# Performance work log

Hardware: AMD Instinct MI355X
Metric: run time of the kernel (lower is better)

The kernel has to match this reference:

```python
import jax, jax.numpy as jnp
import numpy as np

INPUT_DIM, ENC_H, DEC_H, HORIZON = 8, 384, 384, 18
B, L = 1024, 336


def _lstm_layer(xs, Wih, Whh, bih, bhh):
    # xs: [B, L, D] -> outputs [B, L, H], final h [B, H]
    Bv = xs.shape[0]
    Hh = Whh.shape[1]
    def step(carry, x_t):
        h, c = carry
        z = x_t @ Wih.T + h @ Whh.T + bih + bhh  # [B, 4H], gate order i,f,g,o (PyTorch)
        i, f, g, o = jnp.split(z, 4, axis=-1)
        c = jax.nn.sigmoid(f) * c + jax.nn.sigmoid(i) * jnp.tanh(g)
        h = jax.nn.sigmoid(o) * jnp.tanh(c)
        return (h, c), h
    init = (jnp.zeros((Bv, Hh), xs.dtype), jnp.zeros((Bv, Hh), xs.dtype))
    (h, c), ys = jax.lax.scan(step, init, jnp.swapaxes(xs, 0, 1))
    return jnp.swapaxes(ys, 0, 1), h


def setup_inputs() -> dict:
    key = jax.random.key(0)
    ks = jax.random.split(key, 20)
    s = 0.05
    d = {
        "x": jax.random.normal(ks[0], (B, L, INPUT_DIM), jnp.float32),
        "future_feats": jax.random.normal(ks[1], (B, HORIZON, 4), jnp.float32),
        # encoder layer 0
        "enc_Wih0": jax.random.normal(ks[2], (4 * ENC_H, INPUT_DIM), jnp.float32) * s,
        "enc_Whh0": jax.random.normal(ks[3], (4 * ENC_H, ENC_H), jnp.float32) * s,
        "enc_bih0": jax.random.normal(ks[4], (4 * ENC_H,), jnp.float32) * s,
        "enc_bhh0": jax.random.normal(ks[5], (4 * ENC_H,), jnp.float32) * s,
        # encoder layer 1
        "enc_Wih1": jax.random.normal(ks[6], (4 * ENC_H, ENC_H), jnp.float32) * s,
        "enc_Whh1": jax.random.normal(ks[7], (4 * ENC_H, ENC_H), jnp.float32) * s,
        "enc_bih1": jax.random.normal(ks[8], (4 * ENC_H,), jnp.float32) * s,
        "enc_bhh1": jax.random.normal(ks[9], (4 * ENC_H,), jnp.float32) * s,
        # attention projection (no bias)
        "Wa": jax.random.normal(ks[10], (DEC_H, ENC_H), jnp.float32) * s,
        # dec_in: Linear(1+4+enc_h -> dec_h)
        "dec_in_W": jax.random.normal(ks[11], (DEC_H, 1 + 4 + ENC_H), jnp.float32) * s,
        "dec_in_b": jax.random.normal(ks[12], (DEC_H,), jnp.float32) * s,
        # decoder LSTM (1 layer)
        "dec_Wih": jax.random.normal(ks[13], (4 * DEC_H, DEC_H), jnp.float32) * s,
        "dec_Whh": jax.random.normal(ks[14], (4 * DEC_H, DEC_H), jnp.float32) * s,
        "dec_bih": jax.random.normal(ks[15], (4 * DEC_H,), jnp.float32) * s,
        "dec_bhh": jax.random.normal(ks[16], (4 * DEC_H,), jnp.float32) * s,
        # output head
        "out_W": jax.random.normal(ks[17], (1, DEC_H), jnp.float32) * s,
        "out_b": jax.random.normal(ks[18], (1,), jnp.float32) * s,
    }
    return d


def reference(x, future_feats, enc_Wih0, enc_Whh0, enc_bih0, enc_bhh0,
              enc_Wih1, enc_Whh1, enc_bih1, enc_bhh1, Wa, dec_in_W, dec_in_b,
              dec_Wih, dec_Whh, dec_bih, dec_bhh, out_W, out_b):
    Bv = x.shape[0]
    # 2-layer encoder (eval mode: inter-layer dropout inactive)
    h1, _ = _lstm_layer(x, enc_Wih0, enc_Whh0, enc_bih0, enc_bhh0)
    enc_out, h_last = _lstm_layer(h1, enc_Wih1, enc_Whh1, enc_bih1, enc_bhh1)
    proj = enc_out @ Wa.T  # [B, L, dec_h] (Wa(enc_out) is step-invariant)

    def dec_step(carry, feat_t):
        h, c, y_prev = carry
        scores = jnp.einsum('bld,bd->bl', proj, h)
        alpha = jax.nn.softmax(scores, axis=1)
        ctx = jnp.einsum('bl,bld->bd', alpha, enc_out)
        din = jnp.concatenate([y_prev, feat_t, ctx], axis=1)  # [B, 1+4+enc_h]
        din = jax.nn.relu(din @ dec_in_W.T + dec_in_b)
        z = din @ dec_Wih.T + h @ dec_Whh.T + dec_bih + dec_bhh
        i, f, g, o = jnp.split(z, 4, axis=-1)
        c = jax.nn.sigmoid(f) * c + jax.nn.sigmoid(i) * jnp.tanh(g)
        h = jax.nn.sigmoid(o) * jnp.tanh(c)
        y_t = h @ out_W.T + out_b  # [B, 1]
        y_prev = jax.lax.stop_gradient(y_t)  # .detach() in torch
        return (h, c, y_prev), y_t

    init = (h_last, jnp.zeros_like(h_last), jnp.zeros((Bv, 1), x.dtype))
    _, ys = jax.lax.scan(dec_step, init, jnp.swapaxes(future_feats, 0, 1))
    return jnp.swapaxes(ys, 0, 1)  # [B, horizon, 1]
```

## Files before the change

kernel.cpp:

```cpp
#include <hip/hip_runtime.h>
#include <stdint.h>

typedef __bf16 bf16;
typedef __bf16 bf16x8 __attribute__((ext_vector_type(8)));
typedef short  s16x8  __attribute__((ext_vector_type(8)));
typedef float  f32x4  __attribute__((ext_vector_type(4)));
typedef uint32_t u32;

#define NB   1024
#define LSEQ 336
#define HID  384
#define HOR  18
#define SMEM_BYTES 36864

__device__ bf16  g_H0[(size_t)(LSEQ+1)*NB*HID];
__device__ bf16  g_enc[(size_t)NB*LSEQ*HID];
__device__ bf16  g_zero[HID];
__device__ bf16  g_Adec[2*NB*768];
__device__ bf16  g_Adin[NB*416];
__device__ bf16  g_xb[NB*LSEQ*8];
__device__ float g_cdec[NB*HID];
__device__ float g_u[NB*HID];
__device__ float g_bias0[1536], g_bias1[1536], g_biasd[1536], g_biasdin[384];
__device__ bf16  g_Bp0[12*13*4096];
__device__ bf16  g_Bp1n[24*24*4*64*8];
__device__ bf16  g_Bpd[12*24*4096];
__device__ bf16  g_Bpi[3*13*4096];
__device__ bf16  g_Bpu[3*12*4096];
__device__ int   g_f0[8*LSEQ];
__device__ int   g_f1[4*(LSEQ+1)];

__device__ __forceinline__ float sigf(float x){ return 1.0f/(1.0f + __expf(-x)); }
__device__ __forceinline__ float tanh_f(float x){
  x = fminf(fmaxf(x, -15.f), 15.f);
  float e = __expf(2.f*x);
  return (e - 1.f)/(e + 1.f);
}

__device__ __forceinline__ void ds16(bf16* p, s16x8 v){
  union{ s16x8 v; uint64_t q[2]; } u; u.v = v;
  __hip_atomic_store((uint64_t*)p,     u.q[0], __ATOMIC_RELAXED, __HIP_MEMORY_SCOPE_AGENT);
  __hip_atomic_store((uint64_t*)p + 1, u.q[1], __ATOMIC_RELAXED, __HIP_MEMORY_SCOPE_AGENT);
}

__global__ void zero_state_k(){
  int i = blockIdx.x*blockDim.x + threadIdx.x;
  int st = gridDim.x*blockDim.x;
  bf16 z = (bf16)0.f;
  for(int k=i;k<NB*HID;k+=st){ g_H0[k]=z; g_cdec[k]=0.f; }
  for(int k=i;k<8*LSEQ;k+=st) g_f0[k]=0;
  for(int k=i;k<4*(LSEQ+1);k+=st) g_f1[k]=0;
}

__global__ void pack_xb_k(const float* __restrict__ x){
  int i = blockIdx.x*256 + threadIdx.x;
  int n = NB*LSEQ*8;
  for(int k=i; k<n; k+=gridDim.x*256) g_xb[k] = (bf16)x[k];
}

__global__ void pack_gates_k(int mode, const float* __restrict__ W1, const float* __restrict__ W2,
                             int nks){
  bf16* out = (mode==0)? g_Bp0 : g_Bpd;
  size_t idx = (size_t)blockIdx.x*256 + threadIdx.x;
  size_t total = (size_t)12*nks*512;
  if(idx >= total) return;
  int lane = (int)(idx & 63);
  int tt   = (int)((idx>>6) & 7);
  size_t tmp = idx >> 9;
  int ks = (int)(tmp % nks);
  int jb = (int)(tmp / nks);
  int n  = (tt>>1)*HID + jb*32 + (tt&1)*16 + (lane&15);
  int kb = ks*32 + (lane>>4)*8;
  bf16x8 v;
  #pragma unroll
  for(int i=0;i<8;i++){
    int k = kb + i;
    float f;
    if(mode==0) f = (k<384) ? W1[(size_t)n*384 + k] : (k<392 ? W2[(size_t)n*8 + (k-384)] : 0.f);
    else        f = (k<384) ? W1[(size_t)n*384 + k] : W2[(size_t)n*384 + (k-384)];
    v[i] = (bf16)f;
  }
  *(bf16x8*)(out + idx*8) = v;
}

__global__ void pack_gates16_k(const float* __restrict__ Wih1, const float* __restrict__ Whh1){
  int idx = blockIdx.x*256 + threadIdx.x;
  if(idx >= 24*24*4*64) return;
  int lane = idx&63, rem = idx>>6;
  int g = rem&3; rem >>= 2;
  int ks = rem%24, jn = rem/24;
  int n  = g*HID + jn*16 + (lane&15);
  int kb = ks*32 + (lane>>4)*8;
  bf16x8 v;
  #pragma unroll
  for(int i=0;i<8;i++){
    int k = kb+i;
    float f = (k<384)? Wih1[(size_t)n*384 + k] : Whh1[(size_t)n*384 + (k-384)];
    v[i] = (bf16)f;
  }
  *(bf16x8*)(g_Bp1n + (size_t)idx*8) = v;
}

__global__ void pack_plain_k(int mode, const float* __restrict__ W, int nks, int nb_cnt){
  bf16* out = mode ? g_Bpu : g_Bpi;
  size_t idx = (size_t)blockIdx.x*256 + threadIdx.x;
  size_t total = (size_t)nb_cnt*nks*512;
  if(idx>=total) return;
  int lane = (int)(idx&63);
  int tt   = (int)((idx>>6)&7);
  size_t tmp = idx>>9;
  int ks = (int)(tmp%nks);
  int nb = (int)(tmp/nks);
  int n  = nb*128 + tt*16 + (lane&15);
  int kb = ks*32 + (lane>>4)*8;
  bf16x8 v;
  #pragma unroll
  for(int i=0;i<8;i++){
    int k = kb+i;
    float f;
    if(mode==0) f = (k<389)? W[(size_t)n*389 + k] : 0.f;
    else        f = W[(size_t)k*384 + n];
    v[i]=(bf16)f;
  }
  *(bf16x8*)(out + idx*8) = v;
}

__global__ void prep_misc_k(const float* bih0,const float* bhh0,const float* bih1,const float* bhh1,
                            const float* dbih,const float* dbhh,const float* dinb){
  int i = blockIdx.x*256 + threadIdx.x;
  if(i<1536){ g_bias0[i]=bih0[i]+bhh0[i]; g_bias1[i]=bih1[i]+bhh1[i]; g_biasd[i]=dbih[i]+dbhh[i]; }
  if(i<384) g_biasdin[i]=dinb[i];
}

__device__ __forceinline__ void spin_ge(int* p, int tgt){
  while(__hip_atomic_load(p, __ATOMIC_RELAXED, __HIP_MEMORY_SCOPE_AGENT) < tgt){}
}

__global__ __launch_bounds__(256,1)
void enc7_k(){
  extern __shared__ char lds[];
  const int bid = blockIdx.x, tid = threadIdx.x;
  const int lane = tid&63, wv = tid>>6;
  const int l15 = lane&15, lk = (lane>>4)*8;

  if(bid < 96){
    const int g = bid & 7, jb = bid >> 3;
    { const s16x8* src = (const s16x8*)(g_Bp0 + (size_t)jb*13*4096);
      s16x8* dst = (s16x8*)lds;
      #pragma unroll
      for(int h=0;h<26;h++) dst[tid + h*256] = src[tid + h*256];
    }
    bf16* tr = (bf16*)(lds + 13*8192);
    __syncthreads();
    const int jj0 = jb*32 + l15;
    float bia[2],bfa[2],bga[2],boa[2];
    #pragma unroll
    for(int jh=0;jh<2;jh++){
      bia[jh]=g_bias0[jj0+jh*16];     bfa[jh]=g_bias0[384+jj0+jh*16];
      bga[jh]=g_bias0[768+jj0+jh*16]; boa[jh]=g_bias0[1152+jj0+jh*16];
    }
    size_t hoff[2], xoff[2];
    #pragma unroll
    for(int mt=0;mt<2;mt++){
      int row = g*128 + wv*32 + mt*16 + l15;
      hoff[mt] = (size_t)row*HID + lk;
      xoff[mt] = (size_t)row*LSEQ*8;
    }
    float c[2][2][4] = {};
    for(int w=0; w<LSEQ; w++){
      if(tid==0 && w>=1) spin_ge(&g_f0[g*LSEQ + (w-1)], 12);
      __syncthreads();
      asm volatile("" ::: "memory");
      const bf16* H0w = g_H0 + (size_t)w*NB*HID;
      bf16x8 af[13][2];
      #pragma unroll
      for(int ks=0;ks<12;ks++)
        #pragma unroll
        for(int mt=0;mt<2;mt++)
          af[ks][mt] = *(const bf16x8*)(H0w + hoff[mt] + ks*32);
      #pragma unroll
      for(int mt=0;mt<2;mt++){
        bf16x8 z;
        #pragma unroll
        for(int e=0;e<8;e++) z[e]=(bf16)0.f;
        if(lk==0) z = *(const bf16x8*)(g_xb + xoff[mt] + (size_t)w*8);
        af[12][mt] = z;
      }
      f32x4 acc[2][8];
      #pragma unroll
      for(int m2=0;m2<2;m2++)
        #pragma unroll
        for(int tt=0;tt<8;tt++) acc[m2][tt] = (f32x4){0.f,0.f,0.f,0.f};
      #pragma unroll
      for(int ks=0;ks<13;ks++){
        #pragma unroll
        for(int tt=0;tt<8;tt++){
          bf16x8 bfr = *(const bf16x8*)(lds + (ks*8+tt)*1024 + lane*16);
          acc[0][tt] = __builtin_amdgcn_mfma_f32_16x16x32_bf16(af[ks][0], bfr, acc[0][tt],0,0,0);
          acc[1][tt] = __builtin_amdgcn_mfma_f32_16x16x32_bf16(af[ks][1], bfr, acc[1][tt],0,0,0);
        }
      }
      #pragma unroll
      for(int mt=0;mt<2;mt++)
        #pragma unroll
        for(int jh=0;jh<2;jh++)
          #pragma unroll
          for(int r=0;r<4;r++){
            float zi=acc[mt][0+jh][r]+bia[jh], zf=acc[mt][2+jh][r]+bfa[jh],
                  zg=acc[mt][4+jh][r]+bga[jh], zo=acc[mt][6+jh][r]+boa[jh];
            float cn = sigf(zf)*c[mt][jh][r] + sigf(zi)*tanh_f(zg);
            c[mt][jh][r]=cn;
            int lr = wv*32 + mt*16 + (lane>>4)*4 + r;
            tr[lr*32 + jh*16 + l15] = (bf16)(sigf(zo)*tanh_f(cn));
          }
      __syncthreads();
      bf16* H0n = g_H0 + (size_t)(w+1)*NB*HID;
      #pragma unroll
      for(int h=0;h<2;h++){
        int p = tid + h*256;
        int row = p>>2, cc = p&3;
        s16x8 v = *(const s16x8*)(tr + row*32 + cc*8);
        ds16(H0n + (size_t)(g*128+row)*HID + jb*32 + cc*8, v);
      }
      __syncthreads();
      if(tid==0)
        __hip_atomic_fetch_add(&g_f0[g*LSEQ + w], 1, __ATOMIC_RELAXED, __HIP_MEMORY_SCOPE_AGENT);
    }
  } else {
    const int idx = bid-96, m = idx & 3, jn = idx >> 2;
    { const s16x8* src = (const s16x8*)(g_Bp1n + (size_t)jn*24*2048);
      s16x8* dst = (s16x8*)lds;
      #pragma unroll
      for(int h=0;h<24;h++) dst[tid + h*256] = src[tid + h*256];
    }
    bf16* tr = (bf16*)(lds + 24*4096);
    __syncthreads();
    const int jj = jn*16 + l15;
    const float bi=g_bias1[jj], bff=g_bias1[384+jj], bg=g_bias1[768+jj], bo=g_bias1[1152+jj];
    int rows[4]; size_t hoff[4];
    #pragma unroll
    for(int mt=0;mt<4;mt++){
      rows[mt] = m*256 + wv*64 + mt*16 + l15;
      hoff[mt] = (size_t)rows[mt]*HID + lk;
    }
    float c[4][4] = {};
    for(int s=1; s<=LSEQ; s++){
      if(tid==0)           spin_ge(&g_f0[(2*m)*LSEQ + (s-1)], 12);
      else if(tid==1)      spin_ge(&g_f0[(2*m+1)*LSEQ + (s-1)], 12);
      else if(tid==2 && s>=2) spin_ge(&g_f1[m*(LSEQ+1) + (s-1)], 24);
      __syncthreads();
      asm volatile("" ::: "memory");
      const bf16* H0s = g_H0 + (size_t)s*NB*HID;
      const size_t strideE = (s>=2)? (size_t)LSEQ*HID : 0;
      const bf16* Es = (s>=2)? (g_enc + (size_t)(s-2)*HID) : g_zero;
      size_t eoff[4];
      #pragma unroll
      for(int mt=0;mt<4;mt++) eoff[mt] = (size_t)rows[mt]*strideE + lk;
      bf16x8 ap[8][4];
      #pragma unroll
      for(int d=0; d<8; d++)
        #pragma unroll
        for(int mt=0;mt<4;mt++)
          ap[d][mt] = *(const bf16x8*)(H0s + hoff[mt] + d*32);
      f32x4 acc[4][4];
      #pragma unroll
      for(int mt=0;mt<4;mt++)
        #pragma unroll
        for(int g4=0;g4<4;g4++) acc[mt][g4] = (f32x4){0.f,0.f,0.f,0.f};
      #pragma unroll
      for(int ks=0;ks<24;ks++){
        bf16x8 bfr[4];
        #pragma unroll
        for(int g4=0;g4<4;g4++) bfr[g4] = *(const bf16x8*)(lds + (ks*4+g4)*1024 + lane*16);
        bf16x8 a[4];
        #pragma unroll
        for(int mt=0;mt<4;mt++) a[mt] = ap[ks&7][mt];
        int kn = ks+8;
        if(kn<24){
          if(kn<12){
            #pragma unroll
            for(int mt=0;mt<4;mt++) ap[ks&7][mt] = *(const bf16x8*)(H0s + hoff[mt] + kn*32);
          } else {
            #pragma unroll
            for(int mt=0;mt<4;mt++) ap[ks&7][mt] = *(const bf16x8*)(Es + eoff[mt] + (kn-12)*32);
          }
        }
        #pragma unroll
        for(int mt=0;mt<4;mt++)
          #pragma unroll
          for(int g4=0;g4<4;g4++)
            acc[mt][g4] = __builtin_amdgcn_mfma_f32_16x16x32_bf16(a[mt], bfr[g4], acc[mt][g4],0,0,0);
      }
      #pragma unroll
      for(int mt=0;mt<4;mt++)
        #pragma unroll
        for(int r=0;r<4;r++){
          float zi=acc[mt][0][r]+bi, zf=acc[mt][1][r]+bff,
                zg=acc[mt][2][r]+bg, zo=acc[mt][3][r]+bo;
          float cn = sigf(zf)*c[mt][r] + sigf(zi)*tanh_f(zg);
          c[mt][r]=cn;
          int lr = wv*64 + mt*16 + (lane>>4)*4 + r;
          tr[lr*16 + l15] = (bf16)(sigf(zo)*tanh_f(cn));
        }
      __syncthreads();
      const int t = s-1;
      #pragma unroll
      for(int h=0;h<2;h++){
        int p = tid + h*256;
        int row = p>>1, hf2 = p&1;
        s16x8 v = *(const s16x8*)(tr + row*16 + hf2*8);
        ds16(g_enc + ((size_t)(m*256+row)*LSEQ + t)*HID + jn*16 + hf2*8, v);
      }
      __syncthreads();
      if(tid==0)
        __hip_atomic_fetch_add(&g_f1[m*(LSEQ+1) + s], 1, __ATOMIC_RELAXED, __HIP_MEMORY_SCOPE_AGENT);
    }
  }
}

struct SReg { s16x8 a0,a1,b0,b1; };

__device__ __forceinline__ void stage_load(const bf16* __restrict__ A, int ldA,
                                           const bf16* __restrict__ Bk, int tid, SReg& sr){
  int c0 = tid, c1 = tid+256;
  sr.a0 = *(const s16x8*)(A + (size_t)(c0>>2)*ldA + (c0&3)*8);
  sr.a1 = *(const s16x8*)(A + (size_t)(c1>>2)*ldA + (c1&3)*8);
  const s16x8* B8 = (const s16x8*)Bk;
  sr.b0 = B8[c0]; sr.b1 = B8[c1];
}

__device__ __forceinline__ void stage_write(char* Ab, char* Bb, int tid, const SReg& sr){
  int c0 = tid, c1 = tid+256;
  *(s16x8*)(Ab + (c0>>2)*80 + (c0&3)*16) = sr.a0;
  *(s16x8*)(Ab + (c1>>2)*80 + (c1&3)*16) = sr.a1;
  *(s16x8*)(Bb + c0*16) = sr.b0;
  *(s16x8*)(Bb + c1*16) = sr.b1;
}

__device__ __forceinline__ void gemm_core(const bf16* __restrict__ A, int ldA,
                                          const bf16* __restrict__ Bp, int nks,
                                          char* smem, f32x4 acc[4][4]){
  const int tid = threadIdx.x;
  const int lane = tid & 63, wv = tid>>6, wm = wv>>1, wn = wv&1;
  char* Ab0 = smem;            char* Ab1 = smem + 10240;
  char* Bb0 = smem + 20480;    char* Bb1 = smem + 28672;
  f32x4 z = {0.f,0.f,0.f,0.f};
  #pragma unroll
  for(int m=0;m<4;m++)
    #pragma unroll
    for(int g=0;g<4;g++) acc[m][g]=z;
  SReg sr;
  stage_load(A, ldA, Bp, tid, sr);
  stage_write(Ab0, Bb0, tid, sr);
  const int aoff = (wm*64 + (lane&15))*80 + (lane>>4)*16;
  const int boff = wn*1024 + lane*16;
  for(int ks=0; ks<nks; ks++){
    char* Ac = (ks&1)? Ab1: Ab0;
    char* Bc = (ks&1)? Bb1: Bb0;
    char* An = (ks&1)? Ab0: Ab1;
    char* Bn = (ks&1)? Bb0: Bb1;
    bool more = (ks+1)<nks;
    if(more) stage_load(A + (ks+1)*32, ldA, Bp + (size_t)(ks+1)*4096, tid, sr);
    __syncthreads();
    bf16x8 af[4], bfr[4];
    #pragma unroll
    for(int mt=0;mt<4;mt++) af[mt] = *(const bf16x8*)(Ac + aoff + mt*16*80);
    #pragma unroll
    for(int g=0;g<4;g++)    bfr[g] = *(const bf16x8*)(Bc + boff + g*2048);
    #pragma unroll
    for(int mt=0;mt<4;mt++)
      #pragma unroll
      for(int g=0;g<4;g++)
        acc[mt][g] = __builtin_amdgcn_mfma_f32_16x16x32_bf16(af[mt], bfr[g], acc[mt][g], 0,0,0);
    if(more) stage_write(An, Bn, tid, sr);
  }
}

__device__ __forceinline__ void lstm_epi(f32x4 acc[4][4], int mbase, int jb,
     const float* __restrict__ bias, float* __restrict__ cst,
     bf16* __restrict__ d0, int ld0, bf16* __restrict__ d1, size_t ld1){
  int lane = threadIdx.x&63, wv = threadIdx.x>>6, wm = wv>>1, wn = wv&1;
  int j = jb*32 + wn*16 + (lane&15);
  float bi = bias[j], bff = bias[384+j], bg = bias[768+j], bo = bias[1152+j];
  #pragma unroll
  for(int mt=0;mt<4;mt++){
    #pragma unroll
    for(int r=0;r<4;r++){
      int brow = mbase + wm*64 + mt*16 + (lane>>4)*4 + r;
      float zi = acc[mt][0][r]+bi, zf = acc[mt][1][r]+bff,
            zg = acc[mt][2][r]+bg, zo = acc[mt][3][r]+bo;
      size_t ci = (size_t)brow*HID + j;
      float cold = cst[ci];
      float cn = sigf(zf)*cold + sigf(zi)*tanh_f(zg);
      cst[ci] = cn;
      bf16 hb = (bf16)(sigf(zo)*tanh_f(cn));
      d0[(size_t)brow*ld0 + j] = hb;
      if(d1) d1[(size_t)brow*ld1 + j] = hb;
    }
  }
}

__global__ __launch_bounds__(256)
void dec_lstm_k(int t){
  __shared__ char smem[SMEM_BYTES];
  int bid = blockIdx.x, mb = bid/12, jb = bid%12;
  int rs = t&1, wsl = rs^1;
  f32x4 acc[4][4];
  gemm_core(g_Adec + (size_t)rs*NB*768 + (size_t)mb*128*768, 768,
            g_Bpd + (size_t)jb*24*4096, 24, smem, acc);
  lstm_epi(acc, mb*128, jb, g_biasd, g_cdec,
           g_Adec + (size_t)wsl*NB*768 + 384, 768, (bf16*)nullptr, 0);
}

__global__ __launch_bounds__(256)
void plain_gemm_k(int t, int mode, const float* __restrict__ outW,
                  const float* __restrict__ outb, float* __restrict__ out,
                  const float* __restrict__ ff){
  __shared__ char smem[SMEM_BYTES];
  int bid = blockIdx.x, mb = bid/3, nb = bid%3;
  int rs = t&1;
  const bf16* A; int ldA, nks; const bf16* Bp;
  if(mode==1){ A = g_Adec + (size_t)rs*NB*768 + 384; ldA=768; Bp = g_Bpu; nks=12; }
  else       { A = g_Adin;                           ldA=416; Bp = g_Bpi; nks=13; }
  f32x4 acc[4][4];
  gemm_core(A + (size_t)mb*128*ldA, ldA, Bp + (size_t)nb*nks*4096, nks, smem, acc);
  int lane = threadIdx.x&63, wv = threadIdx.x>>6, wm = wv>>1, wn = wv&1;
  bf16* dbf = g_Adec + (size_t)rs*NB*768;
  #pragma unroll
  for(int mt=0;mt<4;mt++){
    #pragma unroll
    for(int ti=0;ti<4;ti++){
      int n = nb*128 + (ti*2+wn)*16 + (lane&15);
      #pragma unroll
      for(int r=0;r<4;r++){
        int brow = mb*128 + wm*64 + mt*16 + (lane>>4)*4 + r;
        float v = acc[mt][ti][r];
        if(mode==0){ v += g_biasdin[n]; v = fmaxf(v,0.f); dbf[(size_t)brow*768 + n] = (bf16)v; }
        else g_u[(size_t)brow*384 + n] = v;
      }
    }
  }
  if(mode==1 && t>=1 && nb==0 && threadIdx.x<128){
    int b = mb*128 + threadIdx.x;
    const s16x8* hp = (const s16x8*)(g_Adec + (size_t)rs*NB*768 + (size_t)b*768 + 384);
    float acc2 = 0.f;
    #pragma unroll 4
    for(int i=0;i<48;i++){
      s16x8 v = hp[i];
      #pragma unroll
      for(int e=0;e<8;e++){
        float hv = __uint_as_float(((u32)(uint16_t)v[e])<<16);
        acc2 += hv*outW[i*8+e];
      }
    }
    float y = acc2 + outb[0];
    out[(size_t)b*HOR + (t-1)] = y;
    g_Adin[(size_t)b*416] = (bf16)y;
    #pragma unroll
    for(int k=0;k<4;k++) g_Adin[(size_t)b*416 + 1 + k] = (bf16)ff[(size_t)b*HOR*4 + t*4 + k];
  }
}

__global__ __launch_bounds__(256)
void attn_k(int t){
  __shared__ float sm[4][392];
  int tid = threadIdx.x, lane = tid&63, w = tid>>6;
  int bl = w>>1, hf = w&1;
  int b = blockIdx.x*2 + bl;
  const float* ub = g_u + (size_t)b*HID + lane*6;
  float u0=ub[0],u1=ub[1],u2=ub[2],u3=ub[3],u4=ub[4],u5=ub[5];
  const u32* er = (const u32*)(g_enc + (size_t)b*LSEQ*HID) + (size_t)hf*168*192 + lane*3;
  int estep = 192;
  if(t & 1){ er += (size_t)167*192; estep = -192; }
  float m=-1e30f, den=0.f, a0=0,a1=0,a2=0,a3=0,a4=0,a5=0;
  for(int l=0;l<168;l++){
    u32 w0 = er[0], w1 = er[1], w2 = er[2];
    er += estep;
    float e0 = __uint_as_float(w0<<16);
    float e1 = __uint_as_float(w0 & 0xffff0000u);
    float e2 = __uint_as_float(w1<<16);
    float e3 = __uint_as_float(w1 & 0xffff0000u);
    float e4 = __uint_as_float(w2<<16);
    float e5 = __uint_as_float(w2 & 0xffff0000u);
    float p = e0*u0 + e1*u1 + e2*u2 + e3*u3 + e4*u4 + e5*u5;
    #pragma unroll
    for(int o=1;o<64;o<<=1) p += __shfl_xor(p, o, 64);
    float mn = fmaxf(m, p);
    float al = __expf(m - mn), pe = __expf(p - mn);
    den = den*al + pe;
    a0 = a0*al + pe*e0; a1 = a1*al + pe*e1; a2 = a2*al + pe*e2;
    a3 = a3*al + pe*e3; a4 = a4*al + pe*e4; a5 = a5*al + pe*e5;
    m = mn;
  }
  if(lane==0){ sm[w][0]=m; sm[w][1]=den; }
  sm[w][2+lane*6+0]=a0; sm[w][2+lane*6+1]=a1; sm[w][2+lane*6+2]=a2;
  sm[w][2+lane*6+3]=a3; sm[w][2+lane*6+4]=a4; sm[w][2+lane*6+5]=a5;
  __syncthreads();
  if(hf==0){
    float m2 = sm[w+1][0], d2 = sm[w+1][1];
    float M = fmaxf(m, m2);
    float f1 = __expf(m - M), f2 = __expf(m2 - M);
    float inv = 1.f/(den*f1 + d2*f2);
    bf16* cd = g_Adin + (size_t)b*416 + 5 + lane*6;
    cd[0] = (bf16)((a0*f1 + sm[w+1][2+lane*6+0]*f2)*inv);
    cd[1] = (bf16)((a1*f1 + sm[w+1][2+lane*6+1]*f2)*inv);
    cd[2] = (bf16)((a2*f1 + sm[w+1][2+lane*6+2]*f2)*inv);
    cd[3] = (bf16)((a3*f1 + sm[w+1][2+lane*6+3]*f2)*inv);
    cd[4] = (bf16)((a4*f1 + sm[w+1][2+lane*6+4]*f2)*inv);
    cd[5] = (bf16)((a5*f1 + sm[w+1][2+lane*6+5]*f2)*inv);
  }
}

__global__ void post_k(int t, const float* __restrict__ outW,
                       const float* __restrict__ outb, float* __restrict__ out){
  int b = blockIdx.x*256 + threadIdx.x;
  if(b>=NB) return;
  int wsl = (t&1)^1;
  const s16x8* hp = (const s16x8*)(g_Adec + (size_t)wsl*NB*768 + (size_t)b*768 + 384);
  float acc = 0.f;
  #pragma unroll 4
  for(int i=0;i<48;i++){
    s16x8 v = hp[i];
    #pragma unroll
    for(int e=0;e<8;e++){
      float hv = __uint_as_float(((u32)(uint16_t)v[e])<<16);
      acc += hv*outW[i*8+e];
    }
  }
  out[(size_t)b*HOR + t] = acc + outb[0];
}

__global__ void dec_prep_k(const float* __restrict__ ff){
  int i = blockIdx.x*256 + threadIdx.x;
  if(i < NB*HID){
    int b = i/HID, j = i%HID;
    g_Adec[(size_t)b*768 + 384 + j] = g_enc[(size_t)b*LSEQ*HID + (size_t)(LSEQ-1)*HID + j];
  }
  if(i < NB*4){
    int b = i>>2, k = i&3;
    g_Adin[(size_t)b*416 + 1 + k] = (bf16)ff[(size_t)b*HOR*4 + k];
  }
  if(i < NB) g_Adin[(size_t)i*416] = (bf16)0.f;
}

extern "C" void kernel_launch(void* const* d_in, const int* in_sizes, int n_in,
                              void* d_out, int out_size, void* d_ws, size_t ws_size,
                              hipStream_t stream){
  const float* x    = (const float*)d_in[0];
  const float* ff   = (const float*)d_in[1];
  const float* Wih0 = (const float*)d_in[2];
  const float* Whh0 = (const float*)d_in[3];
  const float* bih0 = (const float*)d_in[4];
  const float* bhh0 = (const float*)d_in[5];
  const float* Wih1 = (const float*)d_in[6];
  const float* Whh1 = (const float*)d_in[7];
  const float* bih1 = (const float*)d_in[8];
  const float* bhh1 = (const float*)d_in[9];
  const float* Wa   = (const float*)d_in[10];
  const float* dinW = (const float*)d_in[11];
  const float* dinb = (const float*)d_in[12];
  const float* dWih = (const float*)d_in[13];
  const float* dWhh = (const float*)d_in[14];
  const float* dbih = (const float*)d_in[15];
  const float* dbhh = (const float*)d_in[16];
  const float* outW = (const float*)d_in[17];
  const float* outb = (const float*)d_in[18];
  float* out = (float*)d_out;

  zero_state_k<<<1024,256,0,stream>>>();
  pack_xb_k<<<2048,256,0,stream>>>(x);
  pack_gates_k<<<(12*13*512)/256,256,0,stream>>>(0, Whh0, Wih0, 13);
  pack_gates16_k<<<576,256,0,stream>>>(Wih1, Whh1);
  pack_gates_k<<<(12*24*512)/256,256,0,stream>>>(2, dWih, dWhh, 24);
  pack_plain_k<<<(3*13*512)/256,256,0,stream>>>(0, dinW, 13, 3);
  pack_plain_k<<<(3*12*512)/256,256,0,stream>>>(1, Wa, 12, 3);
  prep_misc_k<<<8,256,0,stream>>>(bih0,bhh0,bih1,bhh1,dbih,dbhh,dinb);

  hipFuncSetAttribute((const void*)enc7_k,
                      hipFuncAttributeMaxDynamicSharedMemorySize, 114688);
  enc7_k<<<192,256,114688,stream>>>();

  dec_prep_k<<<1536,256,0,stream>>>(ff);
  for(int t=0;t<HOR;t++){
    plain_gemm_k<<<24,256,0,stream>>>(t, 1, outW, outb, out, ff);
    attn_k<<<512,256,0,stream>>>(t);
    plain_gemm_k<<<24,256,0,stream>>>(t, 0, outW, outb, out, ff);
    dec_lstm_k<<<96,256,0,stream>>>(t);
  }
  post_k<<<4,256,0,stream>>>(17, outW, outb, out);
  (void)in_sizes; (void)n_in; (void)out_size; (void)d_ws; (void)ws_size;
}
```

Baseline: 8.402 ms.

## Stage layer-1 encoder state in compact per-step buffer and overlap dependency wait

Layer-1 hidden outputs are now written to a step-indexed, column-slab-major buffer (g_E1), so the recurrent operand reads of the next step are contiguous instead of strided across the sequence-major g_enc. Blocks copy the previous step's slab into g_enc off the critical path, and the last step is copied after the loop. The wait on the layer-1 flag now happens after the layer-0 operand prefetch, letting those loads overlap the wait. Per-store atomic 64-bit writes are replaced by plain vector stores plus an agent-scope release fence before the flag increment. This adds an extra copy and a large staging buffer, and relies on the fence to keep ordering correct.

```diff
diff --git a/kernel.cpp b/kernel.cpp
--- a/kernel.cpp
+++ b/kernel.cpp
@@ -12,10 +12,11 @@
 #define HID  384
 #define HOR  18
 #define SMEM_BYTES 36864
+#define E1T  ((size_t)24*NB*16)
 
 __device__ bf16  g_H0[(size_t)(LSEQ+1)*NB*HID];
+__device__ bf16  g_E1[(size_t)(LSEQ+1)*E1T];
 __device__ bf16  g_enc[(size_t)NB*LSEQ*HID];
-__device__ bf16  g_zero[HID];
 __device__ bf16  g_Adec[2*NB*768];
 __device__ bf16  g_Adin[NB*416];
 __device__ bf16  g_xb[NB*LSEQ*8];
@@ -37,17 +38,11 @@
   return (e - 1.f)/(e + 1.f);
 }
 
-__device__ __forceinline__ void ds16(bf16* p, s16x8 v){
-  union{ s16x8 v; uint64_t q[2]; } u; u.v = v;
-  __hip_atomic_store((uint64_t*)p,     u.q[0], __ATOMIC_RELAXED, __HIP_MEMORY_SCOPE_AGENT);
-  __hip_atomic_store((uint64_t*)p + 1, u.q[1], __ATOMIC_RELAXED, __HIP_MEMORY_SCOPE_AGENT);
-}
-
 __global__ void zero_state_k(){
   int i = blockIdx.x*blockDim.x + threadIdx.x;
   int st = gridDim.x*blockDim.x;
   bf16 z = (bf16)0.f;
-  for(int k=i;k<NB*HID;k+=st){ g_H0[k]=z; g_cdec[k]=0.f; }
+  for(int k=i;k<NB*HID;k+=st){ g_H0[k]=z; g_E1[k]=z; g_cdec[k]=0.f; }
   for(int k=i;k<8*LSEQ;k+=st) g_f0[k]=0;
   for(int k=i;k<4*(LSEQ+1);k+=st) g_f1[k]=0;
 }
@@ -135,9 +130,12 @@
 __device__ __forceinline__ void spin_ge(int* p, int tgt){
   while(__hip_atomic_load(p, __ATOMIC_RELAXED, __HIP_MEMORY_SCOPE_AGENT) < tgt){}
 }
+__device__ __forceinline__ void release_agent(){
+  __builtin_amdgcn_fence(__ATOMIC_RELEASE, "agent");
+}
 
 __global__ __launch_bounds__(256,1)
-void enc7_k(){
+void enc8_k(){
   extern __shared__ char lds[];
   const int bid = blockIdx.x, tid = threadIdx.x;
   const int lane = tid&63, wv = tid>>6;
@@ -220,11 +218,13 @@
         int p = tid + h*256;
         int row = p>>2, cc = p&3;
         s16x8 v = *(const s16x8*)(tr + row*32 + cc*8);
-        ds16(H0n + (size_t)(g*128+row)*HID + jb*32 + cc*8, v);
+        *(s16x8*)(H0n + (size_t)(g*128+row)*HID + jb*32 + cc*8) = v;
       }
       __syncthreads();
-      if(tid==0)
+      if(tid==0){
+        release_agent();
         __hip_atomic_fetch_add(&g_f0[g*LSEQ + w], 1, __ATOMIC_RELAXED, __HIP_MEMORY_SCOPE_AGENT);
+      }
     }
   } else {
     const int idx = bid-96, m = idx & 3, jn = idx >> 2;
@@ -237,31 +237,31 @@
     __syncthreads();
     const int jj = jn*16 + l15;
     const float bi=g_bias1[jj], bff=g_bias1[384+jj], bg=g_bias1[768+jj], bo=g_bias1[1152+jj];
-    int rows[4]; size_t hoff[4];
+    int rows[4]; size_t hoff[4], eo[4];
+    const int jn_half = (lane>>4)>>1, colin = ((lane>>4)&1)*8;
     #pragma unroll
     for(int mt=0;mt<4;mt++){
       rows[mt] = m*256 + wv*64 + mt*16 + l15;
       hoff[mt] = (size_t)rows[mt]*HID + lk;
+      eo[mt]   = (size_t)jn_half*(NB*16) + (size_t)rows[mt]*16 + colin;
     }
     float c[4][4] = {};
     for(int s=1; s<=LSEQ; s++){
-      if(tid==0)           spin_ge(&g_f0[(2*m)*LSEQ + (s-1)], 12);
-      else if(tid==1)      spin_ge(&g_f0[(2*m+1)*LSEQ + (s-1)], 12);
-      else if(tid==2 && s>=2) spin_ge(&g_f1[m*(LSEQ+1) + (s-1)], 24);
+      if(tid==0)      spin_ge(&g_f0[(2*m)*LSEQ + (s-1)], 12);
+      else if(tid==1) spin_ge(&g_f0[(2*m+1)*LSEQ + (s-1)], 12);
       __syncthreads();
       asm volatile("" ::: "memory");
       const bf16* H0s = g_H0 + (size_t)s*NB*HID;
-      const size_t strideE = (s>=2)? (size_t)LSEQ*HID : 0;
-      const bf16* Es = (s>=2)? (g_enc + (size_t)(s-2)*HID) : g_zero;
-      size_t eoff[4];
-      #pragma unroll
-      for(int mt=0;mt<4;mt++) eoff[mt] = (size_t)rows[mt]*strideE + lk;
+      const bf16* Es  = g_E1 + (size_t)(s-1)*E1T;
       bf16x8 ap[8][4];
       #pragma unroll
       for(int d=0; d<8; d++)
         #pragma unroll
         for(int mt=0;mt<4;mt++)
           ap[d][mt] = *(const bf16x8*)(H0s + hoff[mt] + d*32);
+      if(tid==0 && s>=2) spin_ge(&g_f1[m*(LSEQ+1) + (s-1)], 24);
+      __syncthreads();
+      asm volatile("" ::: "memory");
       f32x4 acc[4][4];
       #pragma unroll
       for(int mt=0;mt<4;mt++)
@@ -282,7 +282,7 @@
             for(int mt=0;mt<4;mt++) ap[ks&7][mt] = *(const bf16x8*)(H0s + hoff[mt] + kn*32);
           } else {
             #pragma unroll
-            for(int mt=0;mt<4;mt++) ap[ks&7][mt] = *(const bf16x8*)(Es + eoff[mt] + (kn-12)*32);
+            for(int mt=0;mt<4;mt++) ap[ks&7][mt] = *(const bf16x8*)(Es + (size_t)(kn-12)*32768 + eo[mt]);
           }
         }
         #pragma unroll
@@ -303,17 +303,45 @@
           tr[lr*16 + l15] = (bf16)(sigf(zo)*tanh_f(cn));
         }
       __syncthreads();
-      const int t = s-1;
+      bf16* E1w = g_E1 + (size_t)s*E1T + (size_t)jn*(NB*16);
       #pragma unroll
       for(int h=0;h<2;h++){
         int p = tid + h*256;
         int row = p>>1, hf2 = p&1;
         s16x8 v = *(const s16x8*)(tr + row*16 + hf2*8);
-        ds16(g_enc + ((size_t)(m*256+row)*LSEQ + t)*HID + jn*16 + hf2*8, v);
+        *(s16x8*)(E1w + (size_t)(m*256+row)*16 + hf2*8) = v;
+      }
+      if((jn&1)==0 && s>=2){
+        const int t_out = s-2;
+        const bf16* Ep = g_E1 + (size_t)(s-1)*E1T;
+        #pragma unroll
+        for(int h=0;h<4;h++){
+          int cch = tid + h*256;
+          int row = cch>>2, seg = cch&3;
+          const bf16* srcp = Ep + (size_t)(jn + (seg>>1))*(NB*16) + (size_t)(m*256+row)*16 + (seg&1)*8;
+          s16x8 v = *(const s16x8*)srcp;
+          *(s16x8*)(g_enc + ((size_t)(m*256+row)*LSEQ + t_out)*HID + jn*16 + seg*8) = v;
+        }
       }
       __syncthreads();
-      if(tid==0)
+      if(tid==0){
+        release_agent();
         __hip_atomic_fetch_add(&g_f1[m*(LSEQ+1) + s], 1, __ATOMIC_RELAXED, __HIP_MEMORY_SCOPE_AGENT);
+      }
+    }
+    if(tid==0) spin_ge(&g_f1[m*(LSEQ+1) + LSEQ], 24);
+    __syncthreads();
+    asm volatile("" ::: "memory");
+    if((jn&1)==0){
+      const bf16* Ep = g_E1 + (size_t)LSEQ*E1T;
+      #pragma unroll
+      for(int h=0;h<4;h++){
+        int cch = tid + h*256;
+        int row = cch>>2, seg = cch&3;
+        const bf16* srcp = Ep + (size_t)(jn + (seg>>1))*(NB*16) + (size_t)(m*256+row)*16 + (seg&1)*8;
+        s16x8 v = *(const s16x8*)srcp;
+        *(s16x8*)(g_enc + ((size_t)(m*256+row)*LSEQ + (LSEQ-1))*HID + jn*16 + seg*8) = v;
+      }
     }
   }
 }
@@ -576,9 +604,9 @@
   pack_plain_k<<<(3*12*512)/256,256,0,stream>>>(1, Wa, 12, 3);
   prep_misc_k<<<8,256,0,stream>>>(bih0,bhh0,bih1,bhh1,dbih,dbhh,dinb);
 
-  hipFuncSetAttribute((const void*)enc7_k,
+  hipFuncSetAttribute((const void*)enc8_k,
                       hipFuncAttributeMaxDynamicSharedMemorySize, 114688);
-  enc7_k<<<192,256,114688,stream>>>();
+  enc8_k<<<192,256,114688,stream>>>();
 
   dec_prep_k<<<1536,256,0,stream>>>(ff);
   for(int t=0;t<HOR;t++){
```

New measurement: 7.944 ms. 1.06x faster.
